# Performance work log

Hardware: AMD Instinct MI355X
Metric: run time of the kernel (lower is better)

## Reference

```python
import jax, jax.numpy as jnp
import numpy as np

K_HOPS = 10
ALPHA = 0.1
N_NODES = 50000
N_EDGES = 600000
F_IN = 128
HIDDEN = 64
N_CLASSES = 40


def setup_inputs() -> dict:
    key = jax.random.key(0)
    k1, k2, k3, k4 = jax.random.split(key, 4)
    x = jax.random.normal(k1, (N_NODES, F_IN), dtype=jnp.float32)
    edge_index = jax.random.randint(k2, (2, N_EDGES), 0, N_NODES, dtype=jnp.int32)
    edge_weight = jnp.ones((N_EDGES,), dtype=jnp.float32)
    W1 = jax.random.normal(k3, (F_IN, HIDDEN), dtype=jnp.float32) * (1.0 / np.sqrt(F_IN))
    b1 = jnp.zeros((HIDDEN,), dtype=jnp.float32)
    W2 = jax.random.normal(k4, (HIDDEN, N_CLASSES), dtype=jnp.float32) * (1.0 / np.sqrt(HIDDEN))
    b2 = jnp.zeros((N_CLASSES,), dtype=jnp.float32)
    return {"x": x, "edge_index": edge_index, "edge_weight": edge_weight,
            "W1": W1, "b1": b1, "W2": W2, "b2": b2}


def reference(x, edge_index, edge_weight, W1, b1, W2, b2):
    n = x.shape[0]
    # GCN symmetric normalization with self-loops (tfg gcn cache)
    self_idx = jnp.arange(n, dtype=edge_index.dtype)
    row = jnp.concatenate([edge_index[0], self_idx])
    col = jnp.concatenate([edge_index[1], self_idx])
    w = jnp.concatenate([edge_weight, jnp.ones((n,), dtype=edge_weight.dtype)])
    deg = jax.ops.segment_sum(w, row, num_segments=n)
    dinv = jnp.where(deg > 0, jax.lax.rsqrt(jnp.maximum(deg, 1e-12)), 0.0)
    nw = dinv[row] * w * dinv[col]  # [E+N] normalized edge weights

    def prop(h):
        # h_out[i] = sum_{(i,j)} nw * h[j]
        return jax.ops.segment_sum(h[col] * nw[:, None], row, num_segments=n)

    def step(h, _):
        h_next = prop(h)
        return h_next, None

    # SSGC: out = (1-alpha)/K * sum_{l=1..K} T^l x + alpha * x
    def step_acc(carry, _):
        h, acc = carry
        h_next = prop(h)
        return (h_next, acc + h_next), None

    (_, acc), _ = jax.lax.scan(step_acc, (x, jnp.zeros_like(x)), None, length=K_HOPS)
    h = (1.0 - ALPHA) / K_HOPS * acc + ALPHA * x  # [N, F]

    h = jax.nn.relu(h @ W1 + b1)  # [N, HIDDEN]
    logits = h @ W2 + b2          # [N, N_CLASSES]
    return logits
```

## Files before the change

kernel.cpp:

```cpp
#include <hip/hip_runtime.h>
#include <hip/hip_fp16.h>
#include <math.h>

constexpr int   N   = 50000;
constexpr int   E   = 600000;
constexpr int   FIN = 128;
constexpr int   H   = 64;
constexpr int   C   = 40;
constexpr int   K   = 10;
constexpr float CK  = (1.0f - 0.1f) / 10.0f;
constexpr float AL  = 0.1f;

typedef float v2f __attribute__((ext_vector_type(2)));

__device__ __forceinline__ unsigned pack_fp8x4(float f0, float f1, float f2, float f3) {
    unsigned r = __builtin_amdgcn_cvt_pk_fp8_f32(f0, f1, 0u, false);
    r = __builtin_amdgcn_cvt_pk_fp8_f32(f2, f3, r, true);
    return r;
}

__device__ __forceinline__ float ep_w(unsigned v) {
    return __half2float(__ushort_as_half((unsigned short)(v >> 16)));
}
__device__ __forceinline__ unsigned ep_pack(int c, float w) {
    return (unsigned)(unsigned short)c |
           ((unsigned)__half_as_ushort(__float2half_rn(w)) << 16);
}

constexpr int G1N  = 64;
constexpr int XPAD = 132;
__global__ __launch_bounds__(256, 2) void k_gemm1(const float* __restrict__ x,
                                                  const float* __restrict__ W1,
                                                  float* __restrict__ y0,
                                                  unsigned char* __restrict__ y0f8) {
    __shared__ float ws[FIN * H];
    __shared__ float xs[G1N * XPAD];
    const float4* W14 = (const float4*)W1;
    const float4* x4  = (const float4*)x;
    int t = threadIdx.x;
    int node0 = blockIdx.x * G1N;
    for (int i = t; i < FIN * H / 4; i += 256) ((float4*)ws)[i] = W14[i];
    for (int p = 0; p < 8; ++p) {
        int idx = p * 256 + t;
        int n   = idx >> 5;
        int kk  = idx & 31;
        int node = node0 + n;
        float4 v = (node < N) ? x4[(size_t)node * (FIN / 4) + kk]
                              : make_float4(0.f, 0.f, 0.f, 0.f);
        *(float4*)(xs + n * XPAD + kk * 4) = v;
    }
    __syncthreads();
    int nb = (t >> 4) * 4;
    int cb = (t & 15) * 4;
    float a00=0,a01=0,a02=0,a03=0, a10=0,a11=0,a12=0,a13=0;
    float a20=0,a21=0,a22=0,a23=0, a30=0,a31=0,a32=0,a33=0;
#pragma unroll 8
    for (int k = 0; k < FIN; ++k) {
        float4 wv = *(const float4*)(ws + k * H + cb);
        float x0 = xs[(nb + 0) * XPAD + k];
        float x1 = xs[(nb + 1) * XPAD + k];
        float x2 = xs[(nb + 2) * XPAD + k];
        float x3 = xs[(nb + 3) * XPAD + k];
        a00 = fmaf(x0, wv.x, a00); a01 = fmaf(x0, wv.y, a01);
        a02 = fmaf(x0, wv.z, a02); a03 = fmaf(x0, wv.w, a03);
        a10 = fmaf(x1, wv.x, a10); a11 = fmaf(x1, wv.y, a11);
        a12 = fmaf(x1, wv.z, a12); a13 = fmaf(x1, wv.w, a13);
        a20 = fmaf(x2, wv.x, a20); a21 = fmaf(x2, wv.y, a21);
        a22 = fmaf(x2, wv.z, a22); a23 = fmaf(x2, wv.w, a23);
        a30 = fmaf(x3, wv.x, a30); a31 = fmaf(x3, wv.y, a31);
        a32 = fmaf(x3, wv.z, a32); a33 = fmaf(x3, wv.w, a33);
    }
    float4 rows[4] = {make_float4(a00,a01,a02,a03), make_float4(a10,a11,a12,a13),
                      make_float4(a20,a21,a22,a23), make_float4(a30,a31,a32,a33)};
#pragma unroll
    for (int i = 0; i < 4; ++i) {
        int node = node0 + nb + i;
        if (node >= N) break;
        float4 r = rows[i];
        *(float4*)(y0 + (size_t)node * H + cb) = r;
        *(unsigned*)(y0f8 + (size_t)node * H + cb) = pack_fp8x4(r.x, r.y, r.z, r.w);
    }
}

__global__ void k_count(const int* __restrict__ row, int* __restrict__ cnt8) {
    int e = blockIdx.x * blockDim.x + threadIdx.x;
    if (e >= E) return;
    atomicAdd(&cnt8[(size_t)(blockIdx.x & 7) * N + row[e]], 1);
}

__global__ __launch_bounds__(1024) void k_scan_blocks(const int* __restrict__ cnt8,
                                                      int* __restrict__ row_ptr,
                                                      int* __restrict__ bsum) {
    __shared__ int s[1024];
    int gid = blockIdx.x * 1024 + threadIdx.x;
    int v = 0;
    if (gid < N) {
#pragma unroll
        for (int c = 0; c < 8; ++c) v += cnt8[(size_t)c * N + gid];
    }
    s[threadIdx.x] = v;
    __syncthreads();
    for (int off = 1; off < 1024; off <<= 1) {
        int t = (threadIdx.x >= off) ? s[threadIdx.x - off] : 0;
        __syncthreads();
        s[threadIdx.x] += t;
        __syncthreads();
    }
    if (gid < N) row_ptr[gid] = s[threadIdx.x] - v;
    if (threadIdx.x == 1023) bsum[blockIdx.x] = s[1023];
}

__global__ void k_scan_sums(const int* __restrict__ bsum, int* __restrict__ boff, int nb) {
    int lane = threadIdx.x;
    int orig = (lane < nb) ? bsum[lane] : 0;
    int v = orig;
    for (int off = 1; off < 64; off <<= 1) {
        int t = __shfl_up(v, off, 64);
        if (lane >= off) v += t;
    }
    if (lane < nb) boff[lane] = v - orig;
}

__global__ __launch_bounds__(1024) void k_addoff(int* __restrict__ row_ptr,
                                                 const int* __restrict__ boff,
                                                 int* __restrict__ cnt8) {
    int gid = blockIdx.x * 1024 + threadIdx.x;
    if (gid < N) {
        int rp = row_ptr[gid] + boff[blockIdx.x];
        row_ptr[gid] = rp;
        int off = rp;
#pragma unroll
        for (int c = 0; c < 8; ++c) {
            int t = cnt8[(size_t)c * N + gid];
            cnt8[(size_t)c * N + gid] = off;
            off += t;
        }
    }
    if (gid == 0) row_ptr[N] = E;
}

__global__ void k_scatter(const int* __restrict__ row, const int* __restrict__ col,
                          const float* __restrict__ w,
                          int* __restrict__ off8, unsigned* __restrict__ ep) {
    int e = blockIdx.x * blockDim.x + threadIdx.x;
    if (e >= E) return;
    int r = row[e];
    int p = atomicAdd(&off8[(size_t)(blockIdx.x & 7) * N + r], 1);
    ep[p] = ep_pack(col[e], w[e]);
}

__global__ void k_deg_dinv(const unsigned* __restrict__ ep, const int* __restrict__ row_ptr,
                           float* __restrict__ dinv, float* __restrict__ dinv2) {
    int i = blockIdx.x * blockDim.x + threadIdx.x;
    if (i >= N) return;
    float d = 1.0f;
    int e0 = row_ptr[i], e1 = row_ptr[i + 1];
    for (int j = e0; j < e1; ++j) d += ep_w(ep[j]);
    float di = rsqrtf(d);
    dinv[i]  = di;
    dinv2[i] = di * di;
}

__global__ __launch_bounds__(256) void k_norm(unsigned* __restrict__ ep,
                                              const int* __restrict__ row_ptr,
                                              const float* __restrict__ dinv) {
    int node = blockIdx.x * 32 + (threadIdx.x >> 3);
    if (node >= N) return;
    int l = threadIdx.x & 7;
    float dr = dinv[node];
    int e0 = row_ptr[node], e1 = row_ptr[node + 1];
    for (int j = e0 + l; j < e1; j += 8) {
        unsigned v = ep[j];
        int c = v & 0xFFFFu;
        ep[j] = ep_pack(c, ep_w(v) * dr * dinv[c]);
    }
}

constexpr int HSP = 68;
template <bool WRITE_H, bool ACC_INIT, bool FINAL>
__global__ __launch_bounds__(256) void k_prop(const uint2* __restrict__ hin,
                                              uint2* __restrict__ hout,
                                              __half* __restrict__ acch,
                                              const float* __restrict__ dinv2,
                                              const int* __restrict__ row_ptr,
                                              const unsigned* __restrict__ ep,
                                              const float4* __restrict__ y04,
                                              const float* __restrict__ b1,
                                              const float* __restrict__ W2,
                                              const float* __restrict__ b2,
                                              float* __restrict__ out) {
    extern __shared__ float smem[];
    float* w2s = smem;
    float* hs  = smem + H * C;
    float* b2s = hs + 32 * HSP;
    float* b1s = b2s + C;
    int t = threadIdx.x;
    if (FINAL) {
        for (int i = t; i < H * C; i += 256) w2s[i] = W2[i];
        if (t < C) b2s[t] = b2[t];
        if (t < H) b1s[t] = b1[t];
        __syncthreads();
    }
    int lane = t & 63;
    int nib  = (t >> 6) * 8 + (lane >> 3);
    int l    = lane & 7;
    int node = blockIdx.x * 32 + nib;
    bool nv  = node < N;
    int nodec = nv ? node : N - 1;
    int start = row_ptr[nodec];
    int deg   = nv ? (row_ptr[nodec + 1] - start) : 0;
    int md = deg;
#pragma unroll
    for (int off = 8; off <= 32; off <<= 1) md = max(md, __shfl_xor(md, off, 64));
    float s[8];
#pragma unroll
    for (int i = 0; i < 8; ++i) s[i] = 0.f;
    auto accum = [&](uint2 v, float w) {
        v2f p0 = __builtin_amdgcn_cvt_pk_f32_fp8(v.x, false);
        v2f p1 = __builtin_amdgcn_cvt_pk_f32_fp8(v.x, true);
        v2f p2 = __builtin_amdgcn_cvt_pk_f32_fp8(v.y, false);
        v2f p3 = __builtin_amdgcn_cvt_pk_f32_fp8(v.y, true);
        s[0] = fmaf(w, p0.x, s[0]); s[1] = fmaf(w, p0.y, s[1]);
        s[2] = fmaf(w, p1.x, s[2]); s[3] = fmaf(w, p1.y, s[3]);
        s[4] = fmaf(w, p2.x, s[4]); s[5] = fmaf(w, p2.y, s[5]);
        s[6] = fmaf(w, p3.x, s[6]); s[7] = fmaf(w, p3.y, s[7]);
    };
    for (int j = 0; j < md; j += 2) {
        bool a0 = j < deg, a1 = j + 1 < deg;
        unsigned e0 = ep[a0 ? start + j     : 0];
        unsigned e1 = ep[a1 ? start + j + 1 : 0];
        uint2 v0 = hin[(size_t)(e0 & 0xFFFFu) * 8 + l];
        uint2 v1 = hin[(size_t)(e1 & 0xFFFFu) * 8 + l];
        float w0 = a0 ? ep_w(e0) : 0.0f;
        float w1 = a1 ? ep_w(e1) : 0.0f;
        accum(v0, w0);
        accum(v1, w1);
    }
    if (nv) {
        size_t base = (size_t)nodec * 8 + l;
        accum(hin[base], dinv2[nodec]);
        if (WRITE_H) {
            uint2 o;
            o.x = pack_fp8x4(s[0], s[1], s[2], s[3]);
            o.y = pack_fp8x4(s[4], s[5], s[6], s[7]);
            hout[base] = o;
        }
        uint4* ap = (uint4*)(acch + (size_t)nodec * H + l * 8);
        if (FINAL) {
            uint4 old = *ap;
            const unsigned* u = (const unsigned*)&old;
#pragma unroll
            for (int d = 0; d < 4; ++d) {
                float2 f = __half22float2(*(__half2*)&u[d]);
                s[2*d+0] += f.x; s[2*d+1] += f.y;
            }
            float4 ya = y04[(size_t)nodec * (H / 4) + 2 * l];
            float4 yb = y04[(size_t)nodec * (H / 4) + 2 * l + 1];
            const float* bp = b1s + l * 8;
            float* hp = hs + nib * HSP + l * 8;
            hp[0] = fmaxf(fmaf(CK, s[0], fmaf(AL, ya.x, bp[0])), 0.f);
            hp[1] = fmaxf(fmaf(CK, s[1], fmaf(AL, ya.y, bp[1])), 0.f);
            hp[2] = fmaxf(fmaf(CK, s[2], fmaf(AL, ya.z, bp[2])), 0.f);
            hp[3] = fmaxf(fmaf(CK, s[3], fmaf(AL, ya.w, bp[3])), 0.f);
            hp[4] = fmaxf(fmaf(CK, s[4], fmaf(AL, yb.x, bp[4])), 0.f);
            hp[5] = fmaxf(fmaf(CK, s[5], fmaf(AL, yb.y, bp[5])), 0.f);
            hp[6] = fmaxf(fmaf(CK, s[6], fmaf(AL, yb.z, bp[6])), 0.f);
            hp[7] = fmaxf(fmaf(CK, s[7], fmaf(AL, yb.w, bp[7])), 0.f);
        } else {
            if (!ACC_INIT) {
                uint4 old = *ap;
                const unsigned* u = (const unsigned*)&old;
#pragma unroll
                for (int d = 0; d < 4; ++d) {
                    float2 f = __half22float2(*(__half2*)&u[d]);
                    s[2*d+0] += f.x; s[2*d+1] += f.y;
                }
            }
            uint4 nvp;
            unsigned* u = (unsigned*)&nvp;
#pragma unroll
            for (int d = 0; d < 4; ++d) {
                __half2 h = __floats2half2_rn(s[2*d+0], s[2*d+1]);
                u[d] = *(unsigned*)&h;
            }
            *ap = nvp;
        }
    }
    if (FINAL) {
        __syncthreads();
        int node0 = blockIdx.x * 32;
        for (int o = t; o < 32 * C; o += 256) {
            int nl = o / C, c = o % C;
            int n2 = node0 + nl;
            if (n2 >= N) continue;
            float v = b2s[c];
            const float* hr = &hs[nl * HSP];
#pragma unroll
            for (int k = 0; k < H; ++k) v = fmaf(hr[k], w2s[k * C + c], v);
            out[n2 * C + c] = v;
        }
    }
}

extern "C" void kernel_launch(void* const* d_in, const int* in_sizes, int n_in,
                              void* d_out, int out_size, void* d_ws, size_t ws_size,
                              hipStream_t stream) {
    const float* x  = (const float*)d_in[0];
    const int*   ei = (const int*)d_in[1];
    const float* ew = (const float*)d_in[2];
    const float* W1 = (const float*)d_in[3];
    const float* b1 = (const float*)d_in[4];
    const float* W2 = (const float*)d_in[5];
    const float* b2 = (const float*)d_in[6];
    float* out = (float*)d_out;

    const int* row = ei;
    const int* col = ei + E;

    char* ws = (char*)d_ws;
    size_t off = 0;
    auto alloc = [&](size_t bytes) -> char* {
        char* p = ws + off;
        off = (off + bytes + 1023) & ~(size_t)1023;
        return p;
    };
    float*         y0   = (float*)alloc((size_t)N * H * 4);
    unsigned char* y0f8 = (unsigned char*)alloc((size_t)N * H);
    unsigned char* ha   = (unsigned char*)alloc((size_t)N * H);
    unsigned char* hb   = (unsigned char*)alloc((size_t)N * H);
    __half*        acch = (__half*)alloc((size_t)N * H * 2);
    int*      cnt8   = (int*)     alloc((size_t)8 * N * 4);
    float*    dinv   = (float*)   alloc((size_t)N * 4);
    float*    dinv2  = (float*)   alloc((size_t)N * 4);
    int*      row_ptr= (int*)     alloc((size_t)(N + 1) * 4);
    int*      bsum   = (int*)     alloc(64 * 4);
    int*      boff   = (int*)     alloc(64 * 4);
    unsigned* ep     = (unsigned*)alloc((size_t)E * 4);

    hipMemsetAsync(cnt8, 0, (size_t)8 * N * 4, stream);

    k_gemm1<<<(N + G1N - 1) / G1N, 256, 0, stream>>>(x, W1, y0, y0f8);

    k_count<<<(E + 255) / 256, 256, 0, stream>>>(row, cnt8);

    constexpr int NB = (N + 1023) / 1024;
    k_scan_blocks<<<NB, 1024, 0, stream>>>(cnt8, row_ptr, bsum);
    k_scan_sums<<<1, 64, 0, stream>>>(bsum, boff, NB);
    k_addoff<<<NB, 1024, 0, stream>>>(row_ptr, boff, cnt8);

    k_scatter<<<(E + 255) / 256, 256, 0, stream>>>(row, col, ew, cnt8, ep);
    k_deg_dinv<<<(N + 255) / 256, 256, 0, stream>>>(ep, row_ptr, dinv, dinv2);
    k_norm<<<(N + 31) / 32, 256, 0, stream>>>(ep, row_ptr, dinv);

    const uint2* hin = (const uint2*)y0f8;
    uint2* bufs[2] = {(uint2*)ha, (uint2*)hb};
    const float4* y04 = (const float4*)y0;
    int grid = (N + 31) / 32;
    size_t smemF = (size_t)(H * C + 32 * HSP + C + H) * 4;
    for (int hop = 0; hop < K; ++hop) {
        uint2* hout = bufs[hop & 1];
        if (hop == 0)
            k_prop<true, true, false><<<grid, 256, 0, stream>>>(hin, hout, acch, dinv2,
                row_ptr, ep, y04, b1, W2, b2, out);
        else if (hop == K - 1)
            k_prop<false, false, true><<<grid, 256, smemF, stream>>>(hin, hout, acch, dinv2,
                row_ptr, ep, y04, b1, W2, b2, out);
        else
            k_prop<true, false, false><<<grid, 256, 0, stream>>>(hin, hout, acch, dinv2,
                row_ptr, ep, y04, b1, W2, b2, out);
        hin = hout;
    }
}
```

Baseline: 331.1 us.

## Fuse edge counting into gemm1, batch scatter per block, nontemporal accumulator access

Folds the per-row edge-count atomics into the first GEMM kernel, so each gemm block also counts 768 edges and one kernel launch disappears. The scatter kernel now handles 768 edges per block with the same grid size, keeping the 8-way counter striping consistent with the count pass. The fp16 accumulator loads and stores in the propagation kernel become nontemporal to reduce cache pollution. The main risk is that the atomics lengthen the GEMM blocks, and that NBLK1*768 must cover E, which it does (782*768 > 600000).

```diff
diff --git a/kernel.cpp b/kernel.cpp
--- a/kernel.cpp
+++ b/kernel.cpp
@@ -12,6 +12,7 @@
 constexpr float AL  = 0.1f;
 
 typedef float v2f __attribute__((ext_vector_type(2)));
+typedef unsigned v4u __attribute__((ext_vector_type(4)));
 
 __device__ __forceinline__ unsigned pack_fp8x4(float f0, float f1, float f2, float f3) {
     unsigned r = __builtin_amdgcn_cvt_pk_fp8_f32(f0, f1, 0u, false);
@@ -28,17 +29,33 @@
 }
 
 constexpr int G1N  = 64;
+constexpr int EPB  = 768;
+constexpr int NBLK1 = (N + G1N - 1) / G1N;
+
 constexpr int XPAD = 132;
 __global__ __launch_bounds__(256, 2) void k_gemm1(const float* __restrict__ x,
                                                   const float* __restrict__ W1,
                                                   float* __restrict__ y0,
-                                                  unsigned char* __restrict__ y0f8) {
+                                                  unsigned char* __restrict__ y0f8,
+                                                  const int* __restrict__ row,
+                                                  int* __restrict__ cnt8) {
     __shared__ float ws[FIN * H];
     __shared__ float xs[G1N * XPAD];
     const float4* W14 = (const float4*)W1;
     const float4* x4  = (const float4*)x;
     int t = threadIdx.x;
     int node0 = blockIdx.x * G1N;
+
+    {
+        size_t cbase = (size_t)(blockIdx.x & 7) * N;
+        int e0 = blockIdx.x * EPB;
+#pragma unroll
+        for (int i = 0; i < EPB / 256; ++i) {
+            int e = e0 + i * 256 + t;
+            if (e < E) atomicAdd(&cnt8[cbase + row[e]], 1);
+        }
+    }
+
     for (int i = t; i < FIN * H / 4; i += 256) ((float4*)ws)[i] = W14[i];
     for (int p = 0; p < 8; ++p) {
         int idx = p * 256 + t;
@@ -82,12 +99,6 @@
     }
 }
 
-__global__ void k_count(const int* __restrict__ row, int* __restrict__ cnt8) {
-    int e = blockIdx.x * blockDim.x + threadIdx.x;
-    if (e >= E) return;
-    atomicAdd(&cnt8[(size_t)(blockIdx.x & 7) * N + row[e]], 1);
-}
-
 __global__ __launch_bounds__(1024) void k_scan_blocks(const int* __restrict__ cnt8,
                                                       int* __restrict__ row_ptr,
                                                       int* __restrict__ bsum) {
@@ -139,14 +150,21 @@
     if (gid == 0) row_ptr[N] = E;
 }
 
-__global__ void k_scatter(const int* __restrict__ row, const int* __restrict__ col,
-                          const float* __restrict__ w,
-                          int* __restrict__ off8, unsigned* __restrict__ ep) {
-    int e = blockIdx.x * blockDim.x + threadIdx.x;
-    if (e >= E) return;
-    int r = row[e];
-    int p = atomicAdd(&off8[(size_t)(blockIdx.x & 7) * N + r], 1);
-    ep[p] = ep_pack(col[e], w[e]);
+__global__ __launch_bounds__(256) void k_scatter(const int* __restrict__ row,
+                                                 const int* __restrict__ col,
+                                                 const float* __restrict__ w,
+                                                 int* __restrict__ off8,
+                                                 unsigned* __restrict__ ep) {
+    size_t cbase = (size_t)(blockIdx.x & 7) * N;
+    int e0 = blockIdx.x * EPB;
+#pragma unroll
+    for (int i = 0; i < EPB / 256; ++i) {
+        int e = e0 + i * 256 + threadIdx.x;
+        if (e >= E) continue;
+        int r = row[e];
+        int p = atomicAdd(&off8[cbase + r], 1);
+        ep[p] = ep_pack(col[e], w[e]);
+    }
 }
 
 __global__ void k_deg_dinv(const unsigned* __restrict__ ep, const int* __restrict__ row_ptr,
@@ -245,13 +263,13 @@
             o.y = pack_fp8x4(s[4], s[5], s[6], s[7]);
             hout[base] = o;
         }
-        uint4* ap = (uint4*)(acch + (size_t)nodec * H + l * 8);
+        v4u* ap = (v4u*)(acch + (size_t)nodec * H + l * 8);
         if (FINAL) {
-            uint4 old = *ap;
-            const unsigned* u = (const unsigned*)&old;
+            v4u old = __builtin_nontemporal_load(ap);
 #pragma unroll
             for (int d = 0; d < 4; ++d) {
-                float2 f = __half22float2(*(__half2*)&u[d]);
+                unsigned ud = old[d];
+                float2 f = __half22float2(*(__half2*)&ud);
                 s[2*d+0] += f.x; s[2*d+1] += f.y;
             }
             float4 ya = y04[(size_t)nodec * (H / 4) + 2 * l];
@@ -268,22 +286,21 @@
             hp[7] = fmaxf(fmaf(CK, s[7], fmaf(AL, yb.w, bp[7])), 0.f);
         } else {
             if (!ACC_INIT) {
-                uint4 old = *ap;
-                const unsigned* u = (const unsigned*)&old;
+                v4u old = __builtin_nontemporal_load(ap);
 #pragma unroll
                 for (int d = 0; d < 4; ++d) {
-                    float2 f = __half22float2(*(__half2*)&u[d]);
+                    unsigned ud = old[d];
+                    float2 f = __half22float2(*(__half2*)&ud);
                     s[2*d+0] += f.x; s[2*d+1] += f.y;
                 }
             }
-            uint4 nvp;
-            unsigned* u = (unsigned*)&nvp;
+            v4u nvp;
 #pragma unroll
             for (int d = 0; d < 4; ++d) {
                 __half2 h = __floats2half2_rn(s[2*d+0], s[2*d+1]);
-                u[d] = *(unsigned*)&h;
+                nvp[d] = *(unsigned*)&h;
             }
-            *ap = nvp;
+            __builtin_nontemporal_store(nvp, ap);
         }
     }
     if (FINAL) {
@@ -337,18 +354,16 @@
     int*      boff   = (int*)     alloc(64 * 4);
     unsigned* ep     = (unsigned*)alloc((size_t)E * 4);
 
-    hipMemsetAsync(cnt8, 0, (size_t)8 * N * 4, stream);
-
-    k_gemm1<<<(N + G1N - 1) / G1N, 256, 0, stream>>>(x, W1, y0, y0f8);
-
-    k_count<<<(E + 255) / 256, 256, 0, stream>>>(row, cnt8);
+    (void)hipMemsetAsync(cnt8, 0, (size_t)8 * N * 4, stream);
+
+    k_gemm1<<<NBLK1, 256, 0, stream>>>(x, W1, y0, y0f8, row, cnt8);
 
     constexpr int NB = (N + 1023) / 1024;
     k_scan_blocks<<<NB, 1024, 0, stream>>>(cnt8, row_ptr, bsum);
     k_scan_sums<<<1, 64, 0, stream>>>(bsum, boff, NB);
     k_addoff<<<NB, 1024, 0, stream>>>(row_ptr, boff, cnt8);
 
-    k_scatter<<<(E + 255) / 256, 256, 0, stream>>>(row, col, ew, cnt8, ep);
+    k_scatter<<<NBLK1, 256, 0, stream>>>(row, col, ew, cnt8, ep);
     k_deg_dinv<<<(N + 255) / 256, 256, 0, stream>>>(ep, row_ptr, dinv, dinv2);
     k_norm<<<(N + 31) / 32, 256, 0, stream>>>(ep, row_ptr, dinv);
 
```

Measured after the change: 340.3 us. 2.8% more time.
